# Performance work log

Measured on AMD Instinct MI355X. Metric: run time of the kernel, lower is better.

Reference implementation:

```python
import jax, jax.numpy as jnp
import numpy as np

XZ = jnp.array([0, 2])
XY = jnp.array([0, 1])
YZ = jnp.array([1, 2])


def _bilinear(plane, uv):
    """plane: (C,R,R) as (C,H,W); uv: (N,2) in [0,1], uv[:,0]->width, uv[:,1]->height.
    Border padding + align_corners=True semantics (grid_sample style)."""
    R = plane.shape[-1]
    xy = jnp.clip(uv, 0.0, 1.0) * (R - 1)
    x, y = xy[:, 0], xy[:, 1]
    x0 = jnp.floor(x)
    y0 = jnp.floor(y)
    x0i = jnp.clip(x0.astype(jnp.int32), 0, R - 1)
    y0i = jnp.clip(y0.astype(jnp.int32), 0, R - 1)
    x1i = jnp.clip(x0i + 1, 0, R - 1)
    y1i = jnp.clip(y0i + 1, 0, R - 1)
    wx = (x - x0)[None, :]  # (1,N)
    wy = (y - y0)[None, :]
    f00 = plane[:, y0i, x0i]  # (C,N)
    f01 = plane[:, y0i, x1i]
    f10 = plane[:, y1i, x0i]
    f11 = plane[:, y1i, x1i]
    top = f00 * (1.0 - wx) + f01 * wx
    bot = f10 * (1.0 - wx) + f11 * wx
    return (top * (1.0 - wy) + bot * wy).T  # (N,C)


def _sample_triplane(p, c_xz, c_xy, c_yz):
    """p: (bs,N,3) in [0,1]; planes: (bs,C,R,R). Returns (bs,N,C) summed over planes."""
    def per_batch(pb, fxz, fxy, fyz):
        return (_bilinear(fxz, pb[:, XZ])
                + _bilinear(fxy, pb[:, XY])
                + _bilinear(fyz, pb[:, YZ]))
    return jax.vmap(per_batch)(p, c_xz, c_xy, c_yz)


def setup_inputs() -> dict:
    key = jax.random.key(0)
    ks = jax.random.split(key, 12)
    bs, ns, C, S, R = 2, 50000, 32, 8, 128
    inp = {
        "query_pos": jax.random.uniform(ks[0], (bs, ns, 3), dtype=jnp.float32),
        "c_xz": jax.random.normal(ks[1], (bs, C, R, R), dtype=jnp.float32),
        "c_xy": jax.random.normal(ks[2], (bs, C, R, R), dtype=jnp.float32),
        "c_yz": jax.random.normal(ks[3], (bs, C, R, R), dtype=jnp.float32),
        # offset weights scaled small so sampled points stay mostly in-bounds
        "W_off": jax.random.normal(ks[4], (C, S * 3), dtype=jnp.float32) * 0.01,
        "b_off": jnp.zeros((S * 3,), dtype=jnp.float32),
        "W_w": jax.random.normal(ks[5], (C, S), dtype=jnp.float32) * 0.1,
        "b_w": jnp.zeros((S,), dtype=jnp.float32),
        "W_v": jax.random.normal(ks[6], (C, C), dtype=jnp.float32) * (1.0 / np.sqrt(C)),
        "b_v": jnp.zeros((C,), dtype=jnp.float32),
        "W_out": jax.random.normal(ks[7], (C, C), dtype=jnp.float32) * (1.0 / np.sqrt(C)),
        "b_out": jnp.zeros((C,), dtype=jnp.float32),
    }
    return inp


def reference(query_pos, c_xz, c_xy, c_yz, W_off, b_off, W_w, b_w, W_v, b_v, W_out, b_out):
    bs, ns, _ = query_pos.shape
    S = W_w.shape[1]
    # round 1: sample tri-plane features at query points
    feature = _sample_triplane(query_pos, c_xz, c_xy, c_yz)  # (bs,ns,C)
    # predict per-query sample offsets and weights
    off = (feature @ W_off + b_off).reshape(bs, ns, S, 3)
    w = (feature @ W_w + b_w).reshape(bs, ns, S, 1)
    pts = off + query_pos[:, :, None, :]  # (bs,ns,S,3)
    # round 2: sample at deformed points
    aux = _sample_triplane(pts.reshape(bs, ns * S, 3), c_xz, c_xy, c_yz)
    v = aux.reshape(bs, ns, S, -1) @ W_v + b_v  # (bs,ns,S,C)
    out = (v * w).sum(-2)                        # weighted reduce over samples
    out = out @ W_out + b_out + feature          # residual
    return out  # (bs,ns,C)
```

## Files before the change

### kernel.cpp

```cpp
#include <hip/hip_runtime.h>
#include <hip/hip_fp16.h>

#define BS 2
#define NS 50000
#define CCH 32
#define RR 128
#define SS 8

typedef float v2f __attribute__((ext_vector_type(2)));
typedef _Float16 h2 __attribute__((ext_vector_type(2)));

#if __has_builtin(__builtin_amdgcn_fdot2)
#define HAVE_DOT2 1
#else
#define HAVE_DOT2 0
#endif


__global__ __launch_bounds__(256)
void prep(const float* __restrict__ cxz,
          const float* __restrict__ cxy,
          const float* __restrict__ cyz,
          const float* __restrict__ Wv, const float* __restrict__ bv,
          const float* __restrict__ Wout,
          unsigned* __restrict__ tp, float* __restrict__ Wc,
          float* __restrict__ bvw) {
    __shared__ float lds[32 * 129];
    int tid = threadIdx.x;
    int row = blockIdx.x;
    if (row < BS * 3 * RR) {
        int y  = row & 127;
        int pl = (row >> 7) % 3;
        int b  = row / 384;
        const float* src = (pl == 0) ? cxz : ((pl == 1) ? cxy : cyz);
        const float* sp = src + (((size_t)(b * CCH)) << 14) + (y << 7);
#pragma unroll
        for (int i = 0; i < 16; ++i) {
            int c = (tid >> 7) + 2 * i;
            int x = tid & 127;
            lds[c * 129 + x] = sp[((size_t)c << 14) + x];
        }
        __syncthreads();
        unsigned* dst = tp + ((size_t)row << 12);
#pragma unroll
        for (int i = 0; i < 16; ++i) {
            int idx = tid + 256 * i;
            int c = idx & 31;
            int x = idx >> 5;
            int x1 = min(x + 1, 127);
            unsigned h0 = __half_as_ushort(__float2half(lds[c * 129 + x]));
            unsigned h1 = __half_as_ushort(__float2half(lds[c * 129 + x1]));
            dst[(x << 5) + c] = h0 | (h1 << 16);
        }
    } else {
        int t = (row - BS * 3 * RR) * 256 + tid;
        int c = t >> 5, j = t & 31;
        float acc = 0.f;
#pragma unroll
        for (int k = 0; k < 32; ++k) acc += Wv[c * 32 + k] * Wout[k * 32 + j];
        Wc[t] = acc;
        if (t < 32) {
            float a2 = 0.f;
#pragma unroll
            for (int k = 0; k < 32; ++k) a2 += bv[k] * Wout[k * 32 + t];
            bvw[t] = a2;
        }
    }
}


struct f4 { v2f lo, hi; };

struct Samp { uint4 u[6]; float wc0, wc1, wr1, wr2; };

__device__ __forceinline__ Samp load_samp(const uint4* __restrict__ P0,
                                          float p0, float p1, float p2) {
    Samp t;
    float x0c = fminf(fmaxf(p0, 0.f), 1.f) * 127.f;
    float x1c = fminf(fmaxf(p1, 0.f), 1.f) * 127.f;
    float x2c = fminf(fmaxf(p2, 0.f), 1.f) * 127.f;
    int i0 = min((int)x0c, 126);
    t.wc0 = x0c - (float)i0;
    int i1 = min((int)x1c, 126);
    t.wc1 = x1c - (float)i1;
    float f1 = floorf(x1c);
    int r10 = (int)f1, r11 = min(r10 + 1, 127);
    t.wr1 = x1c - f1;
    float f2 = floorf(x2c);
    int r20 = (int)f2, r21 = min(r20 + 1, 127);
    t.wr2 = x2c - f2;

    const uint4* Pxz = P0;
    const uint4* Pxy = P0 + (1 << 17);
    const uint4* Pyz = P0 + (2 << 17);
    int c0 = i0 << 3, c1 = i1 << 3;
    int R10 = r10 << 10, R11 = r11 << 10;
    int R20 = r20 << 10, R21 = r21 << 10;
    t.u[0] = Pxz[R20 + c0];  t.u[1] = Pxz[R21 + c0];
    t.u[2] = Pxy[R10 + c0];  t.u[3] = Pxy[R11 + c0];
    t.u[4] = Pyz[R20 + c1];  t.u[5] = Pyz[R21 + c1];
    return t;
}

#if HAVE_DOT2
__device__ __forceinline__ void eval_row(f4& acc, uint4 u, h2 w) {
    acc.lo.x = __builtin_amdgcn_fdot2(__builtin_bit_cast(h2, u.x), w, acc.lo.x, false);
    acc.lo.y = __builtin_amdgcn_fdot2(__builtin_bit_cast(h2, u.y), w, acc.lo.y, false);
    acc.hi.x = __builtin_amdgcn_fdot2(__builtin_bit_cast(h2, u.z), w, acc.hi.x, false);
    acc.hi.y = __builtin_amdgcn_fdot2(__builtin_bit_cast(h2, u.w), w, acc.hi.y, false);
}

__device__ __forceinline__ void eval_plane(f4& acc, uint4 ua, uint4 ub,
                                           float wx, float wy) {
    float wB1 = wx * wy;
    float wB0 = wx - wB1;
    float wA1 = wy - wB1;
    float wA0 = 1.f - wx - wA1;
    h2 w0 = __builtin_bit_cast(h2, __builtin_amdgcn_cvt_pkrtz(wA0, wB0));
    h2 w1 = __builtin_bit_cast(h2, __builtin_amdgcn_cvt_pkrtz(wA1, wB1));
    eval_row(acc, ua, w0);
    eval_row(acc, ub, w1);
}
#else
__device__ __forceinline__ void eval_row(f4& acc, uint4 u, float wA, float wB) {
    __half2 h0 = __builtin_bit_cast(__half2, u.x);
    __half2 h1 = __builtin_bit_cast(__half2, u.y);
    __half2 h2_ = __builtin_bit_cast(__half2, u.z);
    __half2 h3 = __builtin_bit_cast(__half2, u.w);
    acc.lo.x = fmaf(__half2float(h0.y), wB, fmaf(__half2float(h0.x), wA, acc.lo.x));
    acc.lo.y = fmaf(__half2float(h1.y), wB, fmaf(__half2float(h1.x), wA, acc.lo.y));
    acc.hi.x = fmaf(__half2float(h2_.y), wB, fmaf(__half2float(h2_.x), wA, acc.hi.x));
    acc.hi.y = fmaf(__half2float(h3.y), wB, fmaf(__half2float(h3.x), wA, acc.hi.y));
}

__device__ __forceinline__ void eval_plane(f4& acc, uint4 ua, uint4 ub,
                                           float wx, float wy) {
    float wB1 = wx * wy;
    float wB0 = wx - wB1;
    float wA1 = wy - wB1;
    float wA0 = 1.f - wx - wA1;
    eval_row(acc, ua, wA0, wB0);
    eval_row(acc, ub, wA1, wB1);
}
#endif

__device__ __forceinline__ void eval_samp(const Samp& t, f4& acc) {
    eval_plane(acc, t.u[0], t.u[1], t.wc0, t.wr2);
    eval_plane(acc, t.u[2], t.u[3], t.wc0, t.wr1);
    eval_plane(acc, t.u[4], t.u[5], t.wc1, t.wr2);
}

#define GETE(v, idx) (((idx) & 2) ? (((idx) & 1) ? (v).hi.y : (v).hi.x) \
                                  : (((idx) & 1) ? (v).lo.y : (v).lo.x))
#define GETC(v, idx) __shfl(GETE(v, idx), base | ((idx) >> 2), 64)

__global__ __launch_bounds__(256)
void eda_main(const float* __restrict__ qp, const unsigned* __restrict__ tp,
              const float* __restrict__ Woff, const float* __restrict__ boff,
              const float* __restrict__ Ww, const float* __restrict__ bw,
              const float* __restrict__ Wc, const float* __restrict__ bvw,
              const float* __restrict__ bout, float* __restrict__ out) {
    __shared__ float sWcat[32][32];
    __shared__ float sWc2[32][32];
    __shared__ float sbcat[32];
    __shared__ float sbvw[32];
    __shared__ float sbout[32];

    int tid = threadIdx.x;
    int lane = tid & 7;
    int base = tid & 56;
    int b  = blockIdx.x & 1;
    int qi = (blockIdx.x >> 1) * 32 + (tid >> 3);
    int qq = min(qi, NS - 1);

    const float* p = qp + ((size_t)b * NS + qq) * 3;
    float p0 = p[0], p1 = p[1], p2 = p[2];

    const uint4* P0 = (const uint4*)tp + (((size_t)(b * 3)) << 17) + lane;

    Samp fs = load_samp(P0, p0, p1, p2);

    for (int i = tid; i < 1024; i += 256) {
        int k = i >> 5, j = i & 31;
        ((float*)sWcat)[i] = (j < 24) ? Woff[k * 24 + j] : Ww[k * 8 + (j - 24)];
        ((float*)sWc2)[i]  = Wc[i];
    }
    if (tid < 32) {
        sbcat[tid] = (tid < 24) ? boff[tid] : bw[tid - 24];
        sbvw[tid]  = bvw[tid];
        sbout[tid] = bout[tid];
    }
    __syncthreads();

    f4 feat; feat.lo = (v2f){0.f, 0.f}; feat.hi = (v2f){0.f, 0.f};
    eval_samp(fs, feat);

    f4 cat;
    cat.lo.x = sbcat[(lane << 2) + 0]; cat.lo.y = sbcat[(lane << 2) + 1];
    cat.hi.x = sbcat[(lane << 2) + 2]; cat.hi.y = sbcat[(lane << 2) + 3];
#pragma unroll
    for (int k = 0; k < 32; ++k) {
        float fc = GETC(feat, k);
        const v2f* wp = (const v2f*)&sWcat[k][lane << 2];
        v2f fc2 = {fc, fc};
        cat.lo = __builtin_elementwise_fma(fc2, wp[0], cat.lo);
        cat.hi = __builtin_elementwise_fma(fc2, wp[1], cat.hi);
    }

    f4 wa; wa.lo = (v2f){0.f, 0.f}; wa.hi = (v2f){0.f, 0.f};
    float wsum = 0.f;
    float w_cur = GETC(cat, 24);
    Samp cur = load_samp(P0, p0 + GETC(cat, 0), p1 + GETC(cat, 1), p2 + GETC(cat, 2));
    Samp nxt;
    float w_nxt;
#pragma unroll
    for (int s = 0; s < SS; ++s) {
        if (s < SS - 1) {
            w_nxt = GETC(cat, 24 + (s + 1));
            nxt = load_samp(P0, p0 + GETC(cat, 3 * (s + 1) + 0),
                                p1 + GETC(cat, 3 * (s + 1) + 1),
                                p2 + GETC(cat, 3 * (s + 1) + 2));
        }
        f4 aux; aux.lo = (v2f){0.f, 0.f}; aux.hi = (v2f){0.f, 0.f};
        eval_samp(cur, aux);
        v2f w2 = {w_cur, w_cur};
        wa.lo = __builtin_elementwise_fma(w2, aux.lo, wa.lo);
        wa.hi = __builtin_elementwise_fma(w2, aux.hi, wa.hi);
        wsum += w_cur;
        if (s < SS - 1) { cur = nxt; w_cur = w_nxt; }
    }

    f4 o;
    v2f ws2 = {wsum, wsum};
    {
        v2f bo  = {sbout[(lane << 2) + 0], sbout[(lane << 2) + 1]};
        v2f bv2 = {sbvw[(lane << 2) + 0], sbvw[(lane << 2) + 1]};
        o.lo = __builtin_elementwise_fma(ws2, bv2, bo) + feat.lo;
        v2f bo2 = {sbout[(lane << 2) + 2], sbout[(lane << 2) + 3]};
        v2f bv3 = {sbvw[(lane << 2) + 2], sbvw[(lane << 2) + 3]};
        o.hi = __builtin_elementwise_fma(ws2, bv3, bo2) + feat.hi;
    }
#pragma unroll
    for (int k = 0; k < 32; ++k) {
        float wc = GETC(wa, k);
        const v2f* wp = (const v2f*)&sWc2[k][lane << 2];
        v2f wc2 = {wc, wc};
        o.lo = __builtin_elementwise_fma(wc2, wp[0], o.lo);
        o.hi = __builtin_elementwise_fma(wc2, wp[1], o.hi);
    }

    if (qi < NS) {
        float* dst = out + ((size_t)b * NS + qi) * 32 + (lane << 2);
        *(float4*)dst = make_float4(o.lo.x, o.lo.y, o.hi.x, o.hi.y);
    }
}

extern "C" void kernel_launch(void* const* d_in, const int* in_sizes, int n_in,
                              void* d_out, int out_size, void* d_ws, size_t ws_size,
                              hipStream_t stream) {
    const float* qp   = (const float*)d_in[0];
    const float* cxz  = (const float*)d_in[1];
    const float* cxy  = (const float*)d_in[2];
    const float* cyz  = (const float*)d_in[3];
    const float* Woff = (const float*)d_in[4];
    const float* boff = (const float*)d_in[5];
    const float* Ww   = (const float*)d_in[6];
    const float* bw   = (const float*)d_in[7];
    const float* Wv   = (const float*)d_in[8];
    const float* bv   = (const float*)d_in[9];
    const float* Wout = (const float*)d_in[10];
    const float* bout = (const float*)d_in[11];
    float* out = (float*)d_out;

    unsigned* tp = (unsigned*)d_ws;
    float* Wc  = (float*)((char*)d_ws + (size_t)BS * 3 * RR * RR * CCH * 4);
    float* bvw = Wc + 1024;

    prep<<<BS * 3 * RR + 4, 256, 0, stream>>>(cxz, cxy, cyz, Wv, bv, Wout, tp, Wc, bvw);
    int blocks_per_batch = (NS + 31) / 32;
    eda_main<<<2 * blocks_per_batch, 256, 0, stream>>>(qp, tp, Woff, boff, Ww, bw,
                                                       Wc, bvw, bout, out);
}
```

Before: 132.5 us.

## Sort queries by spatial cell before main kernel for gather locality

Adds a histogram, scan and scatter pass that bins query points into a 16^3 spatial grid per batch and builds a permutation. The main kernel then processes queries in cell order and scatters outputs back by original index, so neighbouring threads gather from nearby tri-plane texels and reuse cache lines. This costs three extra launches, atomics on the histogram and scatter, and an indirect load of the permutation. Output writes become non-coalesced scattered stores.

Result: slower. 146.4 us (+10.5%).

```diff
diff --git a/kernel.cpp b/kernel.cpp
--- a/kernel.cpp
+++ b/kernel.cpp
@@ -24,7 +24,7 @@
           const float* __restrict__ Wv, const float* __restrict__ bv,
           const float* __restrict__ Wout,
           unsigned* __restrict__ tp, float* __restrict__ Wc,
-          float* __restrict__ bvw) {
+          float* __restrict__ bvw, int* __restrict__ hist) {
     __shared__ float lds[32 * 129];
     int tid = threadIdx.x;
     int row = blockIdx.x;
@@ -52,7 +52,7 @@
             unsigned h1 = __half_as_ushort(__float2half(lds[c * 129 + x1]));
             dst[(x << 5) + c] = h0 | (h1 << 16);
         }
-    } else {
+    } else if (row < BS * 3 * RR + 4) {
         int t = (row - BS * 3 * RR) * 256 + tid;
         int c = t >> 5, j = t & 31;
         float acc = 0.f;
@@ -65,7 +65,58 @@
             for (int k = 0; k < 32; ++k) a2 += bv[k] * Wout[k * 32 + t];
             bvw[t] = a2;
         }
-    }
+    } else {
+        int t = (row - (BS * 3 * RR + 4)) * 256 + tid;
+        hist[t] = 0;
+    }
+}
+
+__device__ __forceinline__ int cell_of(const float* __restrict__ p) {
+    int c0 = min(max((int)(p[0] * 16.f), 0), 15);
+    int c1 = min(max((int)(p[1] * 16.f), 0), 15);
+    int c2 = min(max((int)(p[2] * 16.f), 0), 15);
+    return c0 | (c1 << 4) | (c2 << 8);
+}
+
+__global__ __launch_bounds__(256)
+void hist_k(const float* __restrict__ qp, int* __restrict__ hist) {
+    int g = blockIdx.x * 256 + threadIdx.x;
+    if (g >= BS * NS) return;
+    int cell = cell_of(qp + (size_t)g * 3);
+    int b = (g >= NS) ? 1 : 0;
+    atomicAdd(&hist[(b << 12) + cell], 1);
+}
+
+__global__ __launch_bounds__(1024)
+void scan_k(int* __restrict__ hist) {
+    __shared__ int s[1024];
+    int t = threadIdx.x;
+    int v[8], sum = 0;
+#pragma unroll
+    for (int i = 0; i < 8; ++i) { v[i] = hist[t * 8 + i]; sum += v[i]; }
+    s[t] = sum;
+    __syncthreads();
+    for (int d = 1; d < 1024; d <<= 1) {
+        int x = 0;
+        if (t >= d) x = s[t - d];
+        __syncthreads();
+        if (t >= d) s[t] += x;
+        __syncthreads();
+    }
+    int run = (t == 0) ? 0 : s[t - 1];
+#pragma unroll
+    for (int i = 0; i < 8; ++i) { hist[t * 8 + i] = run; run += v[i]; }
+}
+
+__global__ __launch_bounds__(256)
+void scatter_k(const float* __restrict__ qp, int* __restrict__ ofs,
+               int* __restrict__ perm) {
+    int g = blockIdx.x * 256 + threadIdx.x;
+    if (g >= BS * NS) return;
+    int cell = cell_of(qp + (size_t)g * 3);
+    int b = (g >= NS) ? 1 : 0;
+    int pos = atomicAdd(&ofs[(b << 12) + cell], 1);
+    perm[pos] = g;
 }
 
 
@@ -156,6 +207,7 @@
 
 __global__ __launch_bounds__(256)
 void eda_main(const float* __restrict__ qp, const unsigned* __restrict__ tp,
+              const int* __restrict__ perm,
               const float* __restrict__ Woff, const float* __restrict__ boff,
               const float* __restrict__ Ww, const float* __restrict__ bw,
               const float* __restrict__ Wc, const float* __restrict__ bvw,
@@ -170,10 +222,11 @@
     int lane = tid & 7;
     int base = tid & 56;
     int b  = blockIdx.x & 1;
-    int qi = (blockIdx.x >> 1) * 32 + (tid >> 3);
-    int qq = min(qi, NS - 1);
-
-    const float* p = qp + ((size_t)b * NS + qq) * 3;
+    int li = (blockIdx.x >> 1) * 32 + (tid >> 3);
+    li = min(li, NS - 1);
+    int g = perm[b * NS + li];
+
+    const float* p = qp + (size_t)g * 3;
     float p0 = p[0], p1 = p[1], p2 = p[2];
 
     const uint4* P0 = (const uint4*)tp + (((size_t)(b * 3)) << 17) + lane;
@@ -249,10 +302,8 @@
         o.hi = __builtin_elementwise_fma(wc2, wp[1], o.hi);
     }
 
-    if (qi < NS) {
-        float* dst = out + ((size_t)b * NS + qi) * 32 + (lane << 2);
-        *(float4*)dst = make_float4(o.lo.x, o.lo.y, o.hi.x, o.hi.y);
-    }
+    float* dst = out + (size_t)g * 32 + (lane << 2);
+    *(float4*)dst = make_float4(o.lo.x, o.lo.y, o.hi.x, o.hi.y);
 }
 
 extern "C" void kernel_launch(void* const* d_in, const int* in_sizes, int n_in,
@@ -275,9 +326,16 @@
     unsigned* tp = (unsigned*)d_ws;
     float* Wc  = (float*)((char*)d_ws + (size_t)BS * 3 * RR * RR * CCH * 4);
     float* bvw = Wc + 1024;
-
-    prep<<<BS * 3 * RR + 4, 256, 0, stream>>>(cxz, cxy, cyz, Wv, bv, Wout, tp, Wc, bvw);
+    int*   hist = (int*)(bvw + 32);
+    int*   perm = hist + 8192;
+
+    prep<<<BS * 3 * RR + 4 + 32, 256, 0, stream>>>(cxz, cxy, cyz, Wv, bv, Wout,
+                                                   tp, Wc, bvw, hist);
+    int qblocks = (BS * NS + 255) / 256;
+    hist_k<<<qblocks, 256, 0, stream>>>(qp, hist);
+    scan_k<<<1, 1024, 0, stream>>>(hist);
+    scatter_k<<<qblocks, 256, 0, stream>>>(qp, hist, perm);
     int blocks_per_batch = (NS + 31) / 32;
-    eda_main<<<2 * blocks_per_batch, 256, 0, stream>>>(qp, tp, Woff, boff, Ww, bw,
-                                                       Wc, bvw, bout, out);
-}
+    eda_main<<<2 * blocks_per_batch, 256, 0, stream>>>(qp, tp, perm, Woff, boff,
+                                                       Ww, bw, Wc, bvw, bout, out);
+}
```

## Deepen sample prefetch to three stages with scheduling barriers

Applied to the files above, without the earlier changes.

The round-2 sample loop now keeps a four-slot ring buffer and issues the gathers three samples ahead instead of one, so more memory loads are in flight while earlier samples are evaluated. Scheduling barriers pin the loads ahead of the dependent math, including after the first-round gather, so the compiler cannot sink them. The cost is more live registers for the extra in-flight samples, which may lower occupancy or cause spills.

After: 143.7 us. 1.08x slower.

```diff
diff --git a/kernel.cpp b/kernel.cpp
--- a/kernel.cpp
+++ b/kernel.cpp
@@ -179,6 +179,7 @@
     const uint4* P0 = (const uint4*)tp + (((size_t)(b * 3)) << 17) + lane;
 
     Samp fs = load_samp(P0, p0, p1, p2);
+    __builtin_amdgcn_sched_barrier(0);
 
     for (int i = tid; i < 1024; i += 256) {
         int k = i >> 5, j = i & 31;
@@ -209,25 +210,29 @@
 
     f4 wa; wa.lo = (v2f){0.f, 0.f}; wa.hi = (v2f){0.f, 0.f};
     float wsum = 0.f;
-    float w_cur = GETC(cat, 24);
-    Samp cur = load_samp(P0, p0 + GETC(cat, 0), p1 + GETC(cat, 1), p2 + GETC(cat, 2));
-    Samp nxt;
-    float w_nxt;
+    Samp buf[4];
+#pragma unroll
+    for (int s = 0; s < 3; ++s)
+        buf[s] = load_samp(P0, p0 + GETC(cat, 3 * s + 0),
+                               p1 + GETC(cat, 3 * s + 1),
+                               p2 + GETC(cat, 3 * s + 2));
+    __builtin_amdgcn_sched_barrier(0);
 #pragma unroll
     for (int s = 0; s < SS; ++s) {
-        if (s < SS - 1) {
-            w_nxt = GETC(cat, 24 + (s + 1));
-            nxt = load_samp(P0, p0 + GETC(cat, 3 * (s + 1) + 0),
-                                p1 + GETC(cat, 3 * (s + 1) + 1),
-                                p2 + GETC(cat, 3 * (s + 1) + 2));
-        }
+        if (s + 3 < SS) {
+            int sp = s + 3;
+            buf[sp & 3] = load_samp(P0, p0 + GETC(cat, 3 * sp + 0),
+                                        p1 + GETC(cat, 3 * sp + 1),
+                                        p2 + GETC(cat, 3 * sp + 2));
+        }
+        __builtin_amdgcn_sched_barrier(0);
         f4 aux; aux.lo = (v2f){0.f, 0.f}; aux.hi = (v2f){0.f, 0.f};
-        eval_samp(cur, aux);
-        v2f w2 = {w_cur, w_cur};
+        eval_samp(buf[s & 3], aux);
+        float w_s = GETC(cat, 24 + s);
+        v2f w2 = {w_s, w_s};
         wa.lo = __builtin_elementwise_fma(w2, aux.lo, wa.lo);
         wa.hi = __builtin_elementwise_fma(w2, aux.hi, wa.hi);
-        wsum += w_cur;
-        if (s < SS - 1) { cur = nxt; w_cur = w_nxt; }
+        wsum += w_s;
     }
 
     f4 o;
```
